# Kernel optimization log

Measured on AMD Instinct MI355X. Metric: run time of the kernel, lower is better.

## Reference

```python
import jax, jax.numpy as jnp
import numpy as np

SCALE = 1.0


def _chamfer_pair(a, b):
    # a: [N,3], b: [M,3] -> (dist1 [N], dist2 [M]) squared NN distances
    # ||a-b||^2 = ||a||^2 + ||b||^2 - 2 a.b
    aa = jnp.sum(a * a, axis=-1)            # [N]
    bb = jnp.sum(b * b, axis=-1)            # [M]
    ab = jnp.einsum('nd,md->nm', a, b)      # [N,M]
    d = aa[:, None] + bb[None, :] - 2.0 * ab
    d = jnp.maximum(d, 0.0)
    return jnp.min(d, axis=1), jnp.min(d, axis=0)


def reference(p1, p2):
    # p1, p2: [B, N, 3]; scale applied before distance, matching the torch module
    a = p1 * SCALE
    b = p2 * SCALE
    dist1, dist2 = jax.vmap(_chamfer_pair)(a, b)  # [B,N], [B,M]
    # per-sample loss = mean(dist1) + mean(dist2); total averaged over batch
    per_sample = jnp.mean(dist1, axis=1) + jnp.mean(dist2, axis=1)  # [B]
    return jnp.mean(per_sample).reshape(1)


def setup_inputs() -> dict:
    key = jax.random.key(0)
    k1, k2 = jax.random.split(key)
    B, N, M = 4, 8192, 8192
    p1 = jax.random.normal(k1, (B, N, 3), dtype=jnp.float32)
    p2 = jax.random.normal(k2, (B, M, 3), dtype=jnp.float32)
    return {"p1": p1, "p2": p2}
```

## Files before the change

### kernel.cpp

```cpp
#include <hip/hip_runtime.h>
#include <math.h>

#define BATCH   4
#define NPTS    8192
#define THREADS 256
#define NQ      (2 * BATCH * NPTS)

static constexpr float SCALE = 1.0f;


template<int TCH, int QPT>
__global__ __launch_bounds__(THREADS, 8)
void chamfer_min_kernel(const float* __restrict__ p1,
                        const float* __restrict__ p2,
                        float* __restrict__ pm,
                        float* __restrict__ acc)
{
    constexpr int CHUNK  = NPTS / TCH;
    constexpr int QPB    = THREADS * QPT;
    constexpr int QTILES = NPTS / QPB;

    if (blockIdx.x == 0 && threadIdx.x < 3) acc[threadIdx.x] = 0.0f;

    __shared__ float4 lds4[CHUNK];

    const int bid = blockIdx.x;
    const int c   = bid % TCH;
    const int qt  = (bid / TCH) % QTILES;
    const int b   = (bid / (TCH * QTILES)) % BATCH;
    const int dir = bid / (TCH * QTILES * BATCH);

    const float* qptr = (dir == 0 ? p1 : p2) + (size_t)b * NPTS * 3;
    const float* tptr = (dir == 0 ? p2 : p1) + (size_t)b * NPTS * 3;

    const float* tsrc = tptr + (size_t)c * CHUNK * 3;
    for (int i = threadIdx.x; i < CHUNK; i += THREADS) {
        const float x = tsrc[3 * i + 0] * SCALE;
        const float y = tsrc[3 * i + 1] * SCALE;
        const float z = tsrc[3 * i + 2] * SCALE;
        const float bb = fmaf(z, z, fmaf(y, y, x * x));
        lds4[i] = make_float4(-2.0f * x, -2.0f * y, -2.0f * z, bb);
    }

    const int t  = threadIdx.x;
    const int q0 = qt * QPB + t;
    float qx[QPT], qy[QPT], qz[QPT], qmin[QPT];
    #pragma unroll
    for (int k = 0; k < QPT; ++k) {
        const int q = q0 + k * THREADS;
        qx[k] = qptr[q * 3 + 0] * SCALE;
        qy[k] = qptr[q * 3 + 1] * SCALE;
        qz[k] = qptr[q * 3 + 2] * SCALE;
        qmin[k] = 3.0e38f;
    }

    __syncthreads();

    for (int j = 0; j < CHUNK; j += 8) {
        #pragma unroll
        for (int i = 0; i < 8; i += 2) {
            const float4 t0 = lds4[j + i];
            const float4 t1 = lds4[j + i + 1];
            #pragma unroll
            for (int k = 0; k < QPT; ++k) {
                float s0 = fmaf(qx[k], t0.x, t0.w);
                s0 = fmaf(qy[k], t0.y, s0);
                s0 = fmaf(qz[k], t0.z, s0);
                float s1 = fmaf(qx[k], t1.x, t1.w);
                s1 = fmaf(qy[k], t1.y, s1);
                s1 = fmaf(qz[k], t1.z, s1);
                qmin[k] = fminf(qmin[k], fminf(s0, s1));
            }
        }
    }

    #pragma unroll
    for (int k = 0; k < QPT; ++k) {
        const float aa = fmaf(qz[k], qz[k], fmaf(qy[k], qy[k], qx[k] * qx[k]));
        const int q = q0 + k * THREADS;
        pm[(size_t)c * NQ + (size_t)(dir * BATCH + b) * NPTS + q] = qmin[k] + aa;
    }
}

template<int TCH>
__global__ __launch_bounds__(512)
void chamfer_reduce_kernel(const float* __restrict__ pm,
                           float* __restrict__ acc,
                           float* __restrict__ out)
{
    const int idx = blockIdx.x * 512 + threadIdx.x;
    float m = 3.0e38f;
    #pragma unroll
    for (int c = 0; c < TCH; ++c)
        m = fminf(m, pm[(size_t)c * NQ + idx]);
    m = fmaxf(m, 0.0f);

    #pragma unroll
    for (int o = 32; o > 0; o >>= 1) m += __shfl_down(m, o, 64);

    __shared__ float red[8];
    const int wave = threadIdx.x >> 6;
    const int lane = threadIdx.x & 63;
    if (lane == 0) red[wave] = m;
    __syncthreads();
    if (threadIdx.x == 0) {
        float s = 0.0f;
        #pragma unroll
        for (int w = 0; w < 8; ++w) s += red[w];
        atomicAdd(&acc[blockIdx.x >> 6], s);
        __threadfence();
        const unsigned tk = atomicAdd(reinterpret_cast<unsigned*>(acc + 2), 1u);
        if (tk == 127) {
            __threadfence();
            const float s0 = atomicAdd(&acc[0], 0.0f);
            const float s1 = atomicAdd(&acc[1], 0.0f);
            out[0] = (s0 + s1) * (1.0f / (float)(BATCH * NPTS));
        }
    }
}

template<int TCH, int QPT>
static void launch_all(const float* p1, const float* p2, float* out,
                       void* d_ws, hipStream_t stream)
{
    constexpr int QTILES = NPTS / (THREADS * QPT);
    float* pm  = (float*)d_ws;
    float* acc = pm + (size_t)TCH * NQ;

    chamfer_min_kernel<TCH, QPT><<<2 * BATCH * QTILES * TCH, THREADS, 0, stream>>>(p1, p2, pm, acc);
    chamfer_reduce_kernel<TCH><<<128, 512, 0, stream>>>(pm, acc, out);
}

extern "C" void kernel_launch(void* const* d_in, const int* in_sizes, int n_in,
                              void* d_out, int out_size, void* d_ws, size_t ws_size,
                              hipStream_t stream) {
    const float* p1 = (const float*)d_in[0];
    const float* p2 = (const float*)d_in[1];
    float* out = (float*)d_out;

    const size_t need64 = (size_t)64 * NQ * sizeof(float) + 64;
    if (ws_size >= need64) {
        launch_all<64, 8>(p1, p2, out, d_ws, stream);
    } else {
        launch_all<32, 4>(p1, p2, out, d_ws, stream);
    }
}
```

Measured before the change: 107.3 us.

## Precompute target float4s in a prep kernel and read them directly from global memory

Adds a prep kernel that converts every target point into a packed (-2x,-2y,-2z,|b|^2) float4 buffer in the workspace once, and zeroes the accumulators. The min kernel no longer stages a chunk into LDS or synchronises. Instead every lane reads the same float4 from global memory, relying on uniform broadcast loads and the cache. This removes the redundant per-block conversion and the barrier, but adds a kernel launch and swaps LDS reads for global or scalar-cache loads in the hot loop. The reduce kernel moves to 256-thread blocks, and the fallback configuration changes QPT to 8.

```diff
diff --git a/kernel.cpp b/kernel.cpp
--- a/kernel.cpp
+++ b/kernel.cpp
@@ -9,20 +9,34 @@
 static constexpr float SCALE = 1.0f;
 
 
+__global__ __launch_bounds__(THREADS)
+void chamfer_prep_kernel(const float* __restrict__ p1,
+                         const float* __restrict__ p2,
+                         float4* __restrict__ tgt4,
+                         float* __restrict__ acc)
+{
+    const int id  = blockIdx.x * THREADS + threadIdx.x;
+    const int dir = id >> 15;
+    const int rem = id & 32767;
+    const float* src = (dir == 0 ? p2 : p1);
+    const float x = src[rem * 3 + 0] * SCALE;
+    const float y = src[rem * 3 + 1] * SCALE;
+    const float z = src[rem * 3 + 2] * SCALE;
+    const float bb = fmaf(z, z, fmaf(y, y, x * x));
+    tgt4[id] = make_float4(-2.0f * x, -2.0f * y, -2.0f * z, bb);
+    if (id < 3) acc[id] = 0.0f;
+}
+
 template<int TCH, int QPT>
 __global__ __launch_bounds__(THREADS, 8)
 void chamfer_min_kernel(const float* __restrict__ p1,
                         const float* __restrict__ p2,
-                        float* __restrict__ pm,
-                        float* __restrict__ acc)
+                        const float4* __restrict__ tgt4,
+                        float* __restrict__ pm)
 {
     constexpr int CHUNK  = NPTS / TCH;
     constexpr int QPB    = THREADS * QPT;
     constexpr int QTILES = NPTS / QPB;
-
-    if (blockIdx.x == 0 && threadIdx.x < 3) acc[threadIdx.x] = 0.0f;
-
-    __shared__ float4 lds4[CHUNK];
 
     const int bid = blockIdx.x;
     const int c   = bid % TCH;
@@ -30,17 +44,9 @@
     const int b   = (bid / (TCH * QTILES)) % BATCH;
     const int dir = bid / (TCH * QTILES * BATCH);
 
-    const float* qptr = (dir == 0 ? p1 : p2) + (size_t)b * NPTS * 3;
-    const float* tptr = (dir == 0 ? p2 : p1) + (size_t)b * NPTS * 3;
-
-    const float* tsrc = tptr + (size_t)c * CHUNK * 3;
-    for (int i = threadIdx.x; i < CHUNK; i += THREADS) {
-        const float x = tsrc[3 * i + 0] * SCALE;
-        const float y = tsrc[3 * i + 1] * SCALE;
-        const float z = tsrc[3 * i + 2] * SCALE;
-        const float bb = fmaf(z, z, fmaf(y, y, x * x));
-        lds4[i] = make_float4(-2.0f * x, -2.0f * y, -2.0f * z, bb);
-    }
+    const float*  qptr = (dir == 0 ? p1 : p2) + (size_t)b * NPTS * 3;
+    const float4* tgt  = tgt4 + (size_t)(dir * BATCH + b) * NPTS
+                              + (size_t)c * CHUNK;
 
     const int t  = threadIdx.x;
     const int q0 = qt * QPB + t;
@@ -54,23 +60,19 @@
         qmin[k] = 3.0e38f;
     }
 
-    __syncthreads();
-
-    for (int j = 0; j < CHUNK; j += 8) {
+    #pragma unroll 8
+    for (int j = 0; j < CHUNK; j += 2) {
+        const float4 t0 = tgt[j];
+        const float4 t1 = tgt[j + 1];
         #pragma unroll
-        for (int i = 0; i < 8; i += 2) {
-            const float4 t0 = lds4[j + i];
-            const float4 t1 = lds4[j + i + 1];
-            #pragma unroll
-            for (int k = 0; k < QPT; ++k) {
-                float s0 = fmaf(qx[k], t0.x, t0.w);
-                s0 = fmaf(qy[k], t0.y, s0);
-                s0 = fmaf(qz[k], t0.z, s0);
-                float s1 = fmaf(qx[k], t1.x, t1.w);
-                s1 = fmaf(qy[k], t1.y, s1);
-                s1 = fmaf(qz[k], t1.z, s1);
-                qmin[k] = fminf(qmin[k], fminf(s0, s1));
-            }
+        for (int k = 0; k < QPT; ++k) {
+            float s0 = fmaf(qx[k], t0.x, t0.w);
+            s0 = fmaf(qy[k], t0.y, s0);
+            s0 = fmaf(qz[k], t0.z, s0);
+            float s1 = fmaf(qx[k], t1.x, t1.w);
+            s1 = fmaf(qy[k], t1.y, s1);
+            s1 = fmaf(qz[k], t1.z, s1);
+            qmin[k] = fminf(qmin[k], fminf(s0, s1));
         }
     }
 
@@ -83,12 +85,12 @@
 }
 
 template<int TCH>
-__global__ __launch_bounds__(512)
+__global__ __launch_bounds__(THREADS)
 void chamfer_reduce_kernel(const float* __restrict__ pm,
                            float* __restrict__ acc,
                            float* __restrict__ out)
 {
-    const int idx = blockIdx.x * 512 + threadIdx.x;
+    const int idx = blockIdx.x * THREADS + threadIdx.x;
     float m = 3.0e38f;
     #pragma unroll
     for (int c = 0; c < TCH; ++c)
@@ -98,19 +100,17 @@
     #pragma unroll
     for (int o = 32; o > 0; o >>= 1) m += __shfl_down(m, o, 64);
 
-    __shared__ float red[8];
+    __shared__ float red[4];
     const int wave = threadIdx.x >> 6;
     const int lane = threadIdx.x & 63;
     if (lane == 0) red[wave] = m;
     __syncthreads();
     if (threadIdx.x == 0) {
-        float s = 0.0f;
-        #pragma unroll
-        for (int w = 0; w < 8; ++w) s += red[w];
-        atomicAdd(&acc[blockIdx.x >> 6], s);
+        const float s = red[0] + red[1] + red[2] + red[3];
+        atomicAdd(&acc[blockIdx.x >> 7], s);
         __threadfence();
         const unsigned tk = atomicAdd(reinterpret_cast<unsigned*>(acc + 2), 1u);
-        if (tk == 127) {
+        if (tk == 255) {
             __threadfence();
             const float s0 = atomicAdd(&acc[0], 0.0f);
             const float s1 = atomicAdd(&acc[1], 0.0f);
@@ -124,11 +124,13 @@
                        void* d_ws, hipStream_t stream)
 {
     constexpr int QTILES = NPTS / (THREADS * QPT);
-    float* pm  = (float*)d_ws;
-    float* acc = pm + (size_t)TCH * NQ;
+    float4* tgt4 = (float4*)d_ws;
+    float*  pm   = (float*)(tgt4 + NQ);
+    float*  acc  = pm + (size_t)TCH * NQ;
 
-    chamfer_min_kernel<TCH, QPT><<<2 * BATCH * QTILES * TCH, THREADS, 0, stream>>>(p1, p2, pm, acc);
-    chamfer_reduce_kernel<TCH><<<128, 512, 0, stream>>>(pm, acc, out);
+    chamfer_prep_kernel<<<NQ / THREADS, THREADS, 0, stream>>>(p1, p2, tgt4, acc);
+    chamfer_min_kernel<TCH, QPT><<<2 * BATCH * QTILES * TCH, THREADS, 0, stream>>>(p1, p2, tgt4, pm);
+    chamfer_reduce_kernel<TCH><<<NQ / THREADS, THREADS, 0, stream>>>(pm, acc, out);
 }
 
 extern "C" void kernel_launch(void* const* d_in, const int* in_sizes, int n_in,
@@ -138,10 +140,11 @@
     const float* p2 = (const float*)d_in[1];
     float* out = (float*)d_out;
 
-    const size_t need64 = (size_t)64 * NQ * sizeof(float) + 64;
+    const size_t need64 = (size_t)NQ * sizeof(float4)
+                        + (size_t)64 * NQ * sizeof(float) + 64;
     if (ws_size >= need64) {
         launch_all<64, 8>(p1, p2, out, d_ws, stream);
     } else {
-        launch_all<32, 4>(p1, p2, out, d_ws, stream);
+        launch_all<32, 8>(p1, p2, out, d_ws, stream);
     }
 }
```

After: 125.6 us. 1.17x slower.
